# Optimization experiments

Hardware: AMD Instinct MI355X
Metric: run time of the kernel (lower is better)

Reference implementation:

```python
import jax, jax.numpy as jnp
import numpy as np

N_ENT = 50000
N_REL = 500
N_EDGE = 800000
H_DIM = 96
BN_EPS = 1e-5


def setup_inputs() -> dict:
    key = jax.random.key(0)
    k1, k2, k3, k4, k5 = jax.random.split(key, 5)
    return {
        "ent_emb": jax.random.normal(k1, (N_ENT, H_DIM), dtype=jnp.float32),
        "rel_emb": jax.random.normal(k2, (N_REL, H_DIM), dtype=jnp.float32),
        "neigh_w": jax.random.normal(k3, (H_DIM, H_DIM), dtype=jnp.float32) * (1.0 / np.sqrt(H_DIM)),
        "bn_gamma": jnp.ones((H_DIM,), dtype=jnp.float32),
        "bn_beta": jnp.zeros((H_DIM,), dtype=jnp.float32),
        "rel_id": jax.random.randint(k4, (N_EDGE,), 0, N_REL, dtype=jnp.int64),
        "dst": jax.random.randint(k5, (N_EDGE,), 0, N_ENT, dtype=jnp.int64),
    }


def reference(ent_emb, rel_emb, neigh_w, bn_gamma, bn_beta, rel_id, dst):
    n_nodes = ent_emb.shape[0]
    # per-edge gather: edge feature = relation embedding  [E, D]
    e = rel_emb[rel_id]
    # e_dot_v: dot of edge feature with destination node embedding  [E]
    score = jnp.sum(e * ent_emb[dst], axis=-1)
    # edge softmax over incoming edges of each destination node
    seg_max = jax.ops.segment_max(score, dst, num_segments=n_nodes)  # [N]
    w = jnp.exp(score - seg_max[dst])                                # [E]
    seg_sum = jax.ops.segment_sum(w, dst, num_segments=n_nodes)      # [N]
    alpha = w / seg_sum[dst]                                         # [E]
    # weighted scatter-sum aggregation into destination nodes  [N, D]
    neigh = jax.ops.segment_sum(e * alpha[:, None], dst, num_segments=n_nodes)
    # linear
    out = neigh @ neigh_w
    # BatchNorm1d (training mode: batch stats over nodes, biased var)
    mu = jnp.mean(out, axis=0)
    var = jnp.mean((out - mu) ** 2, axis=0)
    out = (out - mu) * jax.lax.rsqrt(var + BN_EPS) * bn_gamma + bn_beta
    return jnp.tanh(out)
```

## Files before the change

kernel.cpp:

```cpp
#include <hip/hip_runtime.h>
#include <math.h>

#define N_ENT   50000
#define N_REL   500
#define N_EDGE  800000
#define H       96
#define BN_EPS  1e-5f
#define DEG_CAP 64
#define NCOPY   32
#define NBLK_NODE 2048
#define NGRP    ((N_ENT + 3) / 4)
#define SM_SHIFT 24.0f

#define RELW_BLOCKS ((N_REL * H + 255) / 256)
#define ZERO_N      (N_ENT + NCOPY * 2 * H)
#define ZERO_BLOCKS ((ZERO_N + 255) / 256)

__global__ __launch_bounds__(256) void k_init(
        const float* __restrict__ rel, const float* __restrict__ W,
        float* __restrict__ relW, unsigned* __restrict__ zbase) {
    if (blockIdx.x < RELW_BLOCKS) {
        __shared__ float Ws[H * H];
        for (int i = threadIdx.x; i < H * H; i += 256) Ws[i] = W[i];
        __syncthreads();
        int t = blockIdx.x * 256 + threadIdx.x;
        if (t >= N_REL * H) return;
        int r = t / H;
        int c = t - r * H;
        const float4* rr = (const float4*)(rel + (size_t)r * H);
        float acc = 0.0f;
#pragma unroll
        for (int i = 0; i < H / 4; ++i) {
            float4 a = rr[i];
            acc += a.x * Ws[(4 * i + 0) * H + c];
            acc += a.y * Ws[(4 * i + 1) * H + c];
            acc += a.z * Ws[(4 * i + 2) * H + c];
            acc += a.w * Ws[(4 * i + 3) * H + c];
        }
        relW[t] = acc;
    } else {
        int i = (blockIdx.x - RELW_BLOCKS) * 256 + threadIdx.x;
        if (i < ZERO_N) zbase[i] = 0u;
    }
}

__global__ __launch_bounds__(256) void k_bucket(
        const int* __restrict__ dst, const int* __restrict__ rel_id,
        int* __restrict__ cursor, unsigned short* __restrict__ pay) {
    int e = blockIdx.x * 256 + threadIdx.x;
    if (e >= N_EDGE) return;
    int d = dst[e];
    int r = rel_id[e];
    int p = atomicAdd(cursor + d, 1);
    if (p < DEG_CAP) pay[d * DEG_CAP + p] = (unsigned short)r;
}

__global__ __launch_bounds__(256) void k_node(
        const float* __restrict__ ent, const float* __restrict__ rel,
        const unsigned short* __restrict__ pay, const int* __restrict__ cursor,
        const float* __restrict__ relW, float* __restrict__ out,
        float* __restrict__ bn_part) {
    __shared__ float4 sh_er[4][DEG_CAP / 2];
    __shared__ float  sh_red[4][2 * H];
    int wv   = threadIdx.x >> 6;
    int lane = threadIdx.x & 63;

    float2 bsum = make_float2(0.f, 0.f);
    float2 bsq  = make_float2(0.f, 0.f);

    int grp = blockIdx.x;
    int cnt_c, rid_c;
    {
        int n0 = grp * 4 + wv;
        cnt_c = cursor[n0];
        rid_c = (int)pay[(size_t)n0 * DEG_CAP + lane];
    }
    while (grp < NGRP) {
        int grp_nx = grp + (int)gridDim.x;
        int cnt_nx = 0, rid_nx = 0;
        if (grp_nx < NGRP) {
            int nn = grp_nx * 4 + wv;
            cnt_nx = cursor[nn];
            rid_nx = (int)pay[(size_t)nn * DEG_CAP + lane];
        }
        int n   = grp * 4 + wv;
        int cnt = min(cnt_c, DEG_CAP);
        int myrid = (lane < cnt) ? rid_c : 0;
        int npass = (cnt + 15) >> 4;

        {
            int qd = lane & 3;
            int jj = lane >> 2;
            const float4* er = (const float4*)(ent + (size_t)n * H) + qd * 6;
            float4 e0 = er[0], e1 = er[1], e2 = er[2], e3 = er[3], e4 = er[4], e5 = er[5];
            for (int p = 0; p < npass; ++p) {
                int j = (p << 4) + jj;
                int rid = __shfl(myrid, j);
                bool valid = (j < cnt);
                float part = 0.0f;
                const float4* rr = (const float4*)(rel + (size_t)rid * H) + qd * 6;
                float4 b;
                b = rr[0]; part += e0.x*b.x + e0.y*b.y + e0.z*b.z + e0.w*b.w;
                b = rr[1]; part += e1.x*b.x + e1.y*b.y + e1.z*b.z + e1.w*b.w;
                b = rr[2]; part += e2.x*b.x + e2.y*b.y + e2.z*b.z + e2.w*b.w;
                b = rr[3]; part += e3.x*b.x + e3.y*b.y + e3.z*b.z + e3.w*b.w;
                b = rr[4]; part += e4.x*b.x + e4.y*b.y + e4.z*b.z + e4.w*b.w;
                b = rr[5]; part += e5.x*b.x + e5.y*b.y + e5.z*b.z + e5.w*b.w;
                part += __shfl_xor(part, 1);
                part += __shfl_xor(part, 2);
                if (valid && qd == 0) {
                    float2* wr = (float2*)&sh_er[wv][0];
                    wr[j] = make_float2(__expf(part - SM_SHIFT),
                                        __int_as_float(rid));
                }
            }
        }

        float inv;
        {
            const float2* rd = (const float2*)&sh_er[wv][0];
            float ej = (lane < cnt) ? rd[lane].x : 0.0f;
            float s = ej;
#pragma unroll
            for (int off = 1; off < 64; off <<= 1)
                s += __shfl_xor(s, off);
            inv = (cnt > 0) ? 1.0f / s : 0.0f;
        }

        if (lane < 48) {
            float2 acc = make_float2(0.f, 0.f);
            const float2* relW2 = (const float2*)relW;
            for (int p = 0; p < npass; ++p) {
#pragma unroll
                for (int i = 0; i < 8; ++i) {
                    int k0 = (p << 4) + 2 * i;
                    float4 pr = sh_er[wv][(p << 3) + i];
                    bool v0 = (k0 < cnt), v1 = (k0 + 1 < cnt);
                    float al0 = v0 ? pr.x * inv : 0.0f;
                    float al1 = v1 ? pr.z * inv : 0.0f;
                    int r0 = v0 ? __float_as_int(pr.y) : 0;
                    int r1 = v1 ? __float_as_int(pr.w) : 0;
                    float2 f0 = relW2[r0 * 48 + lane];
                    float2 f1 = relW2[r1 * 48 + lane];
                    acc.x += al0 * f0.x + al1 * f1.x;
                    acc.y += al0 * f0.y + al1 * f1.y;
                }
            }
            ((float2*)(out + (size_t)n * H))[lane] = acc;
            bsum.x += acc.x; bsum.y += acc.y;
            bsq.x  += acc.x * acc.x; bsq.y += acc.y * acc.y;
        }
        grp = grp_nx; cnt_c = cnt_nx; rid_c = rid_nx;
    }

    if (lane < 48) {
        ((float2*)&sh_red[wv][0])[lane] = bsum;
        ((float2*)&sh_red[wv][H])[lane] = bsq;
    }
    __syncthreads();
    int t = threadIdx.x;
    if (t < 2 * H) {
        float tot = sh_red[0][t] + sh_red[1][t] + sh_red[2][t] + sh_red[3][t];
        atomicAdd(bn_part + (blockIdx.x & (NCOPY - 1)) * (2 * H) + t, tot);
    }
}

__device__ __forceinline__ float fast_tanh(float x) {
    return 1.0f - 2.0f / (__expf(2.0f * x) + 1.0f);
}

__global__ __launch_bounds__(256) void k_bnapply(
        float* __restrict__ out, const float* __restrict__ bn_part,
        const float* __restrict__ gamma, const float* __restrict__ beta) {
    __shared__ float sA[H], sB[H];
    int t = threadIdx.x;
    if (t < H) {
        float s = 0.0f, qq = 0.0f;
#pragma unroll
        for (int c = 0; c < NCOPY; ++c) {
            s  += bn_part[c * (2 * H) + t];
            qq += bn_part[c * (2 * H) + H + t];
        }
        const float inv_n = 1.0f / (float)N_ENT;
        float mu = s * inv_n;
        float r  = rsqrtf(qq * inv_n - mu * mu + BN_EPS);
        float gg = gamma[t];
        float a  = r * gg;
        sA[t] = a;
        sB[t] = beta[t] - mu * a;
    }
    __syncthreads();
    int idx = blockIdx.x * 256 + t;
    if (idx >= N_ENT * H / 4) return;
    int c4 = idx % (H / 4);
    float4 v = ((const float4*)out)[idx];
    float4 o;
    o.x = fast_tanh(v.x * sA[4 * c4 + 0] + sB[4 * c4 + 0]);
    o.y = fast_tanh(v.y * sA[4 * c4 + 1] + sB[4 * c4 + 1]);
    o.z = fast_tanh(v.z * sA[4 * c4 + 2] + sB[4 * c4 + 2]);
    o.w = fast_tanh(v.w * sA[4 * c4 + 3] + sB[4 * c4 + 3]);
    ((float4*)out)[idx] = o;
}

extern "C" void kernel_launch(void* const* d_in, const int* in_sizes, int n_in,
                              void* d_out, int out_size, void* d_ws, size_t ws_size,
                              hipStream_t stream) {
    const float* ent   = (const float*)d_in[0];
    const float* rel   = (const float*)d_in[1];
    const float* W     = (const float*)d_in[2];
    const float* gamma = (const float*)d_in[3];
    const float* beta  = (const float*)d_in[4];
    const int* rel_id  = (const int*)d_in[5];
    const int* dst     = (const int*)d_in[6];
    float* out = (float*)d_out;

    float* ws       = (float*)d_ws;
    int*   cursor   = (int*)ws;
    float* bn_part  = ws + N_ENT;
    float* relW     = bn_part + NCOPY * 2 * H;
    unsigned short* pay = (unsigned short*)(relW + N_REL * H);

    k_init<<<RELW_BLOCKS + ZERO_BLOCKS, 256, 0, stream>>>(
        rel, W, relW, (unsigned*)cursor);
    k_bucket<<<(N_EDGE + 255) / 256, 256, 0, stream>>>(dst, rel_id, cursor, pay);
    k_node<<<NBLK_NODE, 256, 0, stream>>>(ent, rel, pay, cursor, relW, out,
                                          bn_part);
    k_bnapply<<<(N_ENT * H / 4 + 255) / 256, 256, 0, stream>>>(
        out, bn_part, gamma, beta);
}
```

Measured before the change: 208.5 us.

## Process sixteen nodes per block with 16-lane subgroups per node

Replaces the persistent grid-stride loop, which handled one node per wavefront, with a one-shot grid of N_ENT/16 blocks. Each 16-lane subgroup now handles one node. Entity rows are staged in padded shared memory, each lane computes a full 96-wide score per edge, and aggregation uses float4 loads of relW split across 8 lanes and two edge slots. The aim is better lane utilisation, since the old code left many lanes idle at average degree 16, and fewer serial passes per node. In exchange, BN partial atomics now run once per block rather than once per persistent block, and each subgroup's loop runs to the maximum degree in its wavefront.

```diff
diff --git a/kernel.cpp b/kernel.cpp
--- a/kernel.cpp
+++ b/kernel.cpp
@@ -8,8 +8,7 @@
 #define BN_EPS  1e-5f
 #define DEG_CAP 64
 #define NCOPY   32
-#define NBLK_NODE 2048
-#define NGRP    ((N_ENT + 3) / 4)
+#define NBLK_NODE (N_ENT / 16)
 #define SM_SHIFT 24.0f
 
 #define RELW_BLOCKS ((N_REL * H + 255) / 256)
@@ -60,107 +59,109 @@
         const unsigned short* __restrict__ pay, const int* __restrict__ cursor,
         const float* __restrict__ relW, float* __restrict__ out,
         float* __restrict__ bn_part) {
-    __shared__ float4 sh_er[4][DEG_CAP / 2];
-    __shared__ float  sh_red[4][2 * H];
+    __shared__ float smem[3712];
+    float2* sh_er  = (float2*)smem;
+    float*  sh_ent = smem + 2112;
     int wv   = threadIdx.x >> 6;
     int lane = threadIdx.x & 63;
-
-    float2 bsum = make_float2(0.f, 0.f);
-    float2 bsq  = make_float2(0.f, 0.f);
-
-    int grp = blockIdx.x;
-    int cnt_c, rid_c;
+    int nw   = lane >> 4;
+    int l    = lane & 15;
+    int n    = blockIdx.x * 16 + wv * 4 + nw;
+    int nb   = blockIdx.x * 16 + wv * 4;
+
     {
-        int n0 = grp * 4 + wv;
-        cnt_c = cursor[n0];
-        rid_c = (int)pay[(size_t)n0 * DEG_CAP + lane];
-    }
-    while (grp < NGRP) {
-        int grp_nx = grp + (int)gridDim.x;
-        int cnt_nx = 0, rid_nx = 0;
-        if (grp_nx < NGRP) {
-            int nn = grp_nx * 4 + wv;
-            cnt_nx = cursor[nn];
-            rid_nx = (int)pay[(size_t)nn * DEG_CAP + lane];
-        }
-        int n   = grp * 4 + wv;
-        int cnt = min(cnt_c, DEG_CAP);
-        int myrid = (lane < cnt) ? rid_c : 0;
-        int npass = (cnt + 15) >> 4;
-
-        {
-            int qd = lane & 3;
-            int jj = lane >> 2;
-            const float4* er = (const float4*)(ent + (size_t)n * H) + qd * 6;
-            float4 e0 = er[0], e1 = er[1], e2 = er[2], e3 = er[3], e4 = er[4], e5 = er[5];
-            for (int p = 0; p < npass; ++p) {
-                int j = (p << 4) + jj;
-                int rid = __shfl(myrid, j);
-                bool valid = (j < cnt);
-                float part = 0.0f;
-                const float4* rr = (const float4*)(rel + (size_t)rid * H) + qd * 6;
-                float4 b;
-                b = rr[0]; part += e0.x*b.x + e0.y*b.y + e0.z*b.z + e0.w*b.w;
-                b = rr[1]; part += e1.x*b.x + e1.y*b.y + e1.z*b.z + e1.w*b.w;
-                b = rr[2]; part += e2.x*b.x + e2.y*b.y + e2.z*b.z + e2.w*b.w;
-                b = rr[3]; part += e3.x*b.x + e3.y*b.y + e3.z*b.z + e3.w*b.w;
-                b = rr[4]; part += e4.x*b.x + e4.y*b.y + e4.z*b.z + e4.w*b.w;
-                b = rr[5]; part += e5.x*b.x + e5.y*b.y + e5.z*b.z + e5.w*b.w;
-                part += __shfl_xor(part, 1);
-                part += __shfl_xor(part, 2);
-                if (valid && qd == 0) {
-                    float2* wr = (float2*)&sh_er[wv][0];
-                    wr[j] = make_float2(__expf(part - SM_SHIFT),
-                                        __int_as_float(rid));
-                }
+        const float2* src = (const float2*)(ent + (size_t)nb * H);
+        float2* dst = (float2*)(sh_ent + wv * 400);
+#pragma unroll
+        for (int i = 0; i < 4; ++i) {
+            int idx = lane + (i << 6);
+            if (idx < 200) {
+                int nd = idx / 50;
+                int el = idx - nd * 50;
+                if (el < 48) dst[nd * 50 + el] = src[nd * 48 + el];
             }
         }
-
-        float inv;
-        {
-            const float2* rd = (const float2*)&sh_er[wv][0];
-            float ej = (lane < cnt) ? rd[lane].x : 0.0f;
-            float s = ej;
-#pragma unroll
-            for (int off = 1; off < 64; off <<= 1)
-                s += __shfl_xor(s, off);
-            inv = (cnt > 0) ? 1.0f / s : 0.0f;
-        }
-
-        if (lane < 48) {
-            float2 acc = make_float2(0.f, 0.f);
-            const float2* relW2 = (const float2*)relW;
-            for (int p = 0; p < npass; ++p) {
-#pragma unroll
-                for (int i = 0; i < 8; ++i) {
-                    int k0 = (p << 4) + 2 * i;
-                    float4 pr = sh_er[wv][(p << 3) + i];
-                    bool v0 = (k0 < cnt), v1 = (k0 + 1 < cnt);
-                    float al0 = v0 ? pr.x * inv : 0.0f;
-                    float al1 = v1 ? pr.z * inv : 0.0f;
-                    int r0 = v0 ? __float_as_int(pr.y) : 0;
-                    int r1 = v1 ? __float_as_int(pr.w) : 0;
-                    float2 f0 = relW2[r0 * 48 + lane];
-                    float2 f1 = relW2[r1 * 48 + lane];
-                    acc.x += al0 * f0.x + al1 * f1.x;
-                    acc.y += al0 * f0.y + al1 * f1.y;
-                }
-            }
-            ((float2*)(out + (size_t)n * H))[lane] = acc;
-            bsum.x += acc.x; bsum.y += acc.y;
-            bsq.x  += acc.x * acc.x; bsq.y += acc.y * acc.y;
-        }
-        grp = grp_nx; cnt_c = cnt_nx; rid_c = rid_nx;
-    }
-
-    if (lane < 48) {
-        ((float2*)&sh_red[wv][0])[lane] = bsum;
-        ((float2*)&sh_red[wv][H])[lane] = bsq;
+    }
+
+    int cnt = min(cursor[n], DEG_CAP);
+    int cmx = cnt;
+    cmx = max(cmx, __shfl_xor(cmx, 16));
+    cmx = max(cmx, __shfl_xor(cmx, 32));
+    int npass = (cmx + 15) >> 4;
+    int nstep = (cmx + 1) >> 1;
+
+    float dsum = 0.0f;
+    const float4* en = (const float4*)(sh_ent + wv * 400 + nw * 100);
+    for (int p = 0; p < npass; ++p) {
+        int j = (p << 4) + l;
+        int rid = (int)pay[(size_t)n * DEG_CAP + j];
+        bool valid = (j < cnt);
+        rid = valid ? rid : 0;
+        const float4* rr = (const float4*)(rel + (size_t)rid * H);
+        float p0 = 0.0f, p1 = 0.0f;
+#pragma unroll
+        for (int c = 0; c < H / 4; c += 2) {
+            float4 a0 = en[c],     b0 = rr[c];
+            float4 a1 = en[c + 1], b1 = rr[c + 1];
+            p0 += a0.x*b0.x + a0.y*b0.y + a0.z*b0.z + a0.w*b0.w;
+            p1 += a1.x*b1.x + a1.y*b1.y + a1.z*b1.z + a1.w*b1.w;
+        }
+        float e = valid ? __expf(p0 + p1 - SM_SHIFT) : 0.0f;
+        sh_er[wv * 264 + nw * 66 + j] = make_float2(e, __int_as_float(rid));
+        dsum += e;
+    }
+
+    float s = dsum;
+    s += __shfl_xor(s, 1);
+    s += __shfl_xor(s, 2);
+    s += __shfl_xor(s, 4);
+    s += __shfl_xor(s, 8);
+    float inv = (cnt > 0) ? 1.0f / s : 0.0f;
+
+    int es2 = l >> 3, g = l & 7;
+    float4 A0 = make_float4(0.f, 0.f, 0.f, 0.f), A1 = A0, A2 = A0;
+    for (int st = 0; st < nstep; ++st) {
+        int k = (st << 1) + es2;
+        float2 pr = sh_er[wv * 264 + nw * 66 + k];
+        bool v = (k < cnt);
+        float al = v ? pr.x * inv : 0.0f;
+        int rid = v ? __float_as_int(pr.y) : 0;
+        const float4* fp = (const float4*)(relW + (size_t)rid * H + g * 12);
+        float4 f0 = fp[0], f1 = fp[1], f2 = fp[2];
+        A0.x += al * f0.x; A0.y += al * f0.y; A0.z += al * f0.z; A0.w += al * f0.w;
+        A1.x += al * f1.x; A1.y += al * f1.y; A1.z += al * f1.z; A1.w += al * f1.w;
+        A2.x += al * f2.x; A2.y += al * f2.y; A2.z += al * f2.z; A2.w += al * f2.w;
+    }
+    A0.x += __shfl_xor(A0.x, 8); A0.y += __shfl_xor(A0.y, 8);
+    A0.z += __shfl_xor(A0.z, 8); A0.w += __shfl_xor(A0.w, 8);
+    A1.x += __shfl_xor(A1.x, 8); A1.y += __shfl_xor(A1.y, 8);
+    A1.z += __shfl_xor(A1.z, 8); A1.w += __shfl_xor(A1.w, 8);
+    A2.x += __shfl_xor(A2.x, 8); A2.y += __shfl_xor(A2.y, 8);
+    A2.z += __shfl_xor(A2.z, 8); A2.w += __shfl_xor(A2.w, 8);
+
+    if (l < 8) {
+        float4* op = (float4*)(out + (size_t)n * H + g * 12);
+        op[0] = A0; op[1] = A1; op[2] = A2;
+    }
+
+    __syncthreads();
+    float* sh_red = smem;
+    if (l < 8) {
+        int wid = wv * 4 + nw;
+        float4* ps = (float4*)(sh_red + wid * (2 * H) + g * 12);
+        ps[0] = A0; ps[1] = A1; ps[2] = A2;
+        float4 Q0 = make_float4(A0.x*A0.x, A0.y*A0.y, A0.z*A0.z, A0.w*A0.w);
+        float4 Q1 = make_float4(A1.x*A1.x, A1.y*A1.y, A1.z*A1.z, A1.w*A1.w);
+        float4 Q2 = make_float4(A2.x*A2.x, A2.y*A2.y, A2.z*A2.z, A2.w*A2.w);
+        float4* pq = (float4*)(sh_red + wid * (2 * H) + H + g * 12);
+        pq[0] = Q0; pq[1] = Q1; pq[2] = Q2;
     }
     __syncthreads();
     int t = threadIdx.x;
     if (t < 2 * H) {
-        float tot = sh_red[0][t] + sh_red[1][t] + sh_red[2][t] + sh_red[3][t];
+        float tot = 0.0f;
+#pragma unroll
+        for (int b = 0; b < 16; ++b) tot += sh_red[b * (2 * H) + t];
         atomicAdd(bn_part + (blockIdx.x & (NCOPY - 1)) * (2 * H) + t, tot);
     }
 }
```

Result: slower. 223.4 us (+7.2%).
